# Kernel optimization log

Measured on AMD Instinct MI355X. Metric: run time of the kernel, lower is better.

The kernel has to match this reference:

```python
import jax, jax.numpy as jnp
import numpy as np

N_EMB = 1024
N_HEAD = 16
HEAD_DIM = N_EMB // N_HEAD


def setup_inputs() -> dict:
    key = jax.random.key(0)
    k_x, k_wa, k_ba, k_wp, k_bp = jax.random.split(key, 5)
    B, S = 4, 2048
    scale = 1.0 / np.sqrt(N_EMB)
    return {
        "x": jax.random.normal(k_x, (B, S, N_EMB), dtype=jnp.float32),
        "W_attn": jax.random.normal(k_wa, (N_EMB, 3 * N_EMB), dtype=jnp.float32) * scale,
        "b_attn": jax.random.normal(k_ba, (3 * N_EMB,), dtype=jnp.float32) * 0.01,
        "W_proj": jax.random.normal(k_wp, (N_EMB, N_EMB), dtype=jnp.float32) * scale,
        "b_proj": jax.random.normal(k_bp, (N_EMB,), dtype=jnp.float32) * 0.01,
    }


def _attention(x, W_attn, b_attn, W_proj, b_proj):
    B, S, E = x.shape
    qkv = x @ W_attn + b_attn  # [B, S, 3E]
    q, k, v = jnp.split(qkv, 3, axis=-1)
    # [B, H, S, D]
    q = q.reshape(B, S, N_HEAD, HEAD_DIM).transpose(0, 2, 1, 3)
    k = k.reshape(B, S, N_HEAD, HEAD_DIM).transpose(0, 2, 1, 3)
    v = v.reshape(B, S, N_HEAD, HEAD_DIM).transpose(0, 2, 1, 3)
    scores = jnp.einsum("bhqd,bhkd->bhqk", q, k) / jnp.sqrt(jnp.asarray(HEAD_DIM, x.dtype))
    causal = jnp.tril(jnp.ones((S, S), dtype=bool))
    scores = jnp.where(causal, scores, jnp.asarray(-jnp.inf, x.dtype))
    probs = jax.nn.softmax(scores, axis=-1)
    y = jnp.einsum("bhqk,bhkd->bhqd", probs, v)  # [B, H, S, D]
    y = y.transpose(0, 2, 1, 3).reshape(B, S, E)
    return y @ W_proj + b_proj


def reference(x, W_attn, b_attn, W_proj, b_proj):
    return _attention(x, W_attn, b_attn, W_proj, b_proj)
```

## Files before the change

### kernel.cpp

```cpp
#include <hip/hip_runtime.h>
#include <hip/hip_bf16.h>

typedef __bf16 bf16x8 __attribute__((ext_vector_type(8)));
typedef __bf16 bf16x4 __attribute__((ext_vector_type(4)));
typedef float f32x4 __attribute__((ext_vector_type(4)));

#define MFMA16(a, b, c) __builtin_amdgcn_mfma_f32_16x16x32_bf16(a, b, c, 0, 0, 0)

#define BATCH 4
#define SEQ   2048
#define EMB   1024
#define NHEAD 16
#define HDIM  64
#define ROWS  (BATCH * SEQ)
#define N_QKV (3 * EMB)
#define BH_STRIDE (SEQ * HDIM)

__device__ __forceinline__ void gload_lds16(const __bf16* gp, __bf16* lp) {
  __builtin_amdgcn_global_load_lds(
      (const __attribute__((address_space(1))) void*)gp,
      (__attribute__((address_space(3))) void*)lp, 16, 0, 0);
}

__global__ void cast_f32_to_bf16_x4(const float* __restrict__ src,
                                    __bf16* __restrict__ dst, int n4) {
  int i = blockIdx.x * blockDim.x + threadIdx.x;
  if (i >= n4) return;
  float4 f = ((const float4*)src)[i];
  bf16x4 o;
  o.x = (__bf16)f.x; o.y = (__bf16)f.y; o.z = (__bf16)f.z; o.w = (__bf16)f.w;
  ((bf16x4*)dst)[i] = o;
}

__global__ void transpose_to_bf16(const float* __restrict__ src,
                                  __bf16* __restrict__ dst, int R, int C) {
  __shared__ float t[32][33];
  int c0 = blockIdx.x * 32, r0 = blockIdx.y * 32;
  int tx = threadIdx.x, ty = threadIdx.y;
#pragma unroll
  for (int i = 0; i < 32; i += 8)
    t[ty + i][tx] = src[(size_t)(r0 + ty + i) * C + c0 + tx];
  __syncthreads();
#pragma unroll
  for (int i = 0; i < 32; i += 8)
    dst[(size_t)(c0 + ty + i) * R + r0 + tx] = (__bf16)t[tx][ty + i];
}

__global__ __launch_bounds__(256) void gemm_qkv(
    const __bf16* __restrict__ A, const __bf16* __restrict__ Bt,
    const float* __restrict__ bias,
    __bf16* __restrict__ Qt, __bf16* __restrict__ Kt, __bf16* __restrict__ Vt) {
  const int K = EMB;
  __shared__ __align__(16) __bf16 sA[128 * 32];
  __shared__ __align__(16) __bf16 sB[128 * 32];
  int id = blockIdx.x;
  int xcd = id & 7, j5 = id >> 3;
  int by = j5 >> 3;
  int bx = xcd * 8 + (j5 & 7);
  int m0 = by * 128, n0 = bx * 128;
  int tid = threadIdx.x;
  int wave = tid >> 6, lane = tid & 63;
  int wr = wave >> 1, wc = wave & 1;
  int l16 = lane & 15, quad = lane >> 4, quad4 = quad * 4;
  int f1 = tid * 8;
  int r1 = f1 >> 5, c1 = f1 & 31;
  int f2 = f1 + 2048;
  int r2 = f2 >> 5, c2 = f2 & 31;
  f32x4 acc[4][4] = {};
  for (int k0 = 0; k0 < K; k0 += 32) {
    gload_lds16(A + (size_t)(m0 + r1) * K + k0 + c1, &sA[wave * 512]);
    gload_lds16(A + (size_t)(m0 + r2) * K + k0 + c2, &sA[2048 + wave * 512]);
    gload_lds16(Bt + (size_t)(n0 + r1) * K + k0 + c1, &sB[wave * 512]);
    gload_lds16(Bt + (size_t)(n0 + r2) * K + k0 + c2, &sB[2048 + wave * 512]);
    __syncthreads();
    bf16x8 a[4], b[4];
#pragma unroll
    for (int i = 0; i < 4; i++)
      a[i] = *(const bf16x8*)(sA + (wr * 64 + i * 16 + l16) * 32 + quad * 8);
#pragma unroll
    for (int j = 0; j < 4; j++)
      b[j] = *(const bf16x8*)(sB + (wc * 64 + j * 16 + l16) * 32 + quad * 8);
#pragma unroll
    for (int i = 0; i < 4; i++)
#pragma unroll
      for (int j = 0; j < 4; j++) acc[i][j] = MFMA16(a[i], b[j], acc[i][j]);
    __syncthreads();
  }
  const float KSC = 0.18033688011112043f;
  int sec = m0 >> 10;
#pragma unroll
  for (int i = 0; i < 4; i++) {
    int e0 = m0 + wr * 64 + i * 16 + quad4;
    float4 bv4 = *(const float4*)(bias + e0);
    int h = (e0 & 1023) >> 6, d0 = e0 & 63;
#pragma unroll
    for (int j = 0; j < 4; j++) {
      int scol = n0 + wc * 64 + j * 16 + l16;
      int bidx = scol >> 11, s = scol & 2047;
      size_t base = (size_t)(bidx * NHEAD + h) * BH_STRIDE;
      float v0 = acc[i][j][0] + bv4.x;
      float v1 = acc[i][j][1] + bv4.y;
      float v2 = acc[i][j][2] + bv4.z;
      float v3 = acc[i][j][3] + bv4.w;
      if (sec == 0) {
        int idx = (s >> 4) * 1024 + (d0 >> 5) * 512 + ((d0 >> 3) & 3) * 128 +
                  (s & 15) * 8 + (d0 & 7);
        bf16x4 o4;
        o4.x = (__bf16)(v0 * KSC); o4.y = (__bf16)(v1 * KSC);
        o4.z = (__bf16)(v2 * KSC); o4.w = (__bf16)(v3 * KSC);
        *(bf16x4*)(Qt + base + idx) = o4;
      } else if (sec == 1) {
        int idx = (s >> 6) * 4096 + ((s >> 4) & 3) * 1024 + (d0 >> 5) * 512 +
                  ((d0 >> 3) & 3) * 128 + (s & 15) * 8 + (d0 & 7);
        bf16x4 o4;
        o4.x = (__bf16)v0; o4.y = (__bf16)v1;
        o4.z = (__bf16)v2; o4.w = (__bf16)v3;
        *(bf16x4*)(Kt + base + idx) = o4;
      } else {
        int idx = (s >> 6) * 4096 + (d0 >> 4) * 1024 + ((s >> 5) & 1) * 512 +
                  ((s >> 3) & 3) * 128 + (s & 7) + quad4 * 8;
        Vt[base + idx] = (__bf16)v0;
        Vt[base + idx + 8] = (__bf16)v1;
        Vt[base + idx + 16] = (__bf16)v2;
        Vt[base + idx + 24] = (__bf16)v3;
      }
    }
  }
}

#define PS2 68
__global__ __launch_bounds__(256, 4) void attn_fwd(
    const __bf16* __restrict__ Qt, const __bf16* __restrict__ Kt,
    const __bf16* __restrict__ Vt, __bf16* __restrict__ Y) {
  __shared__ __align__(16) __bf16 sK[4096];
  __shared__ __align__(16) __bf16 sV[4096];
  __shared__ __align__(16) __bf16 pbuf[4][32 * PS2];
  int id = blockIdx.x;
  int g = id >> 6;
  int gg = g & 3, sel = g >> 2;
  int qb = sel == 0 ? gg : sel == 1 ? 15 - gg : sel == 2 ? 4 + gg : 11 - gg;
  int hb = id & 63;
  int h = hb >> 2, b = hb & 3;
  int tid = threadIdx.x;
  int wave = tid >> 6, lane = tid & 63;
  int l16 = lane & 15, quad = lane >> 4, quad4 = quad * 4;
  int q0 = qb * 128;
  size_t bh = (size_t)b * NHEAD + h;
  const __bf16* Qh = Qt + bh * BH_STRIDE;
  const __bf16* Kh = Kt + bh * BH_STRIDE;
  const __bf16* Vh = Vt + bh * BH_STRIDE;
  int mq = q0 + wave * 32;
  const __bf16* qbase = Qh + (size_t)(mq >> 4) * 1024 + lane * 8;
  bf16x8 qa0 = *(const bf16x8*)(qbase);
  bf16x8 qa1 = *(const bf16x8*)(qbase + 512);
  bf16x8 qb0 = *(const bf16x8*)(qbase + 1024);
  bf16x8 qb1 = *(const bf16x8*)(qbase + 1536);
  f32x4 accA[4] = {}, accB[4] = {};
  float lA = 0.f, lB = 0.f;
  const float NEG_INF = -__builtin_inff();
  __bf16* pwA = pbuf[wave];
  __bf16* pwB = pbuf[wave] + 16 * PS2;
  int kt_end = q0 + 128;
  for (int kt = 0; kt < kt_end; kt += 64) {
    const __bf16* kg = Kh + (size_t)(kt >> 6) * 4096 + tid * 8;
    const __bf16* vg = Vh + (size_t)(kt >> 6) * 4096 + tid * 8;
    gload_lds16(kg, sK + tid * 8);
    gload_lds16(kg + 2048, sK + 2048 + tid * 8);
    gload_lds16(vg, sV + tid * 8);
    gload_lds16(vg + 2048, sV + 2048 + tid * 8);
    __syncthreads();
    bool diag = (kt + 64 > mq);
    int relA = mq + l16 - kt;
#pragma unroll
    for (int t = 0; t < 4; t++) {
      bf16x8 ka = *(const bf16x8*)(sK + t * 1024 + lane * 8);
      bf16x8 kb = *(const bf16x8*)(sK + t * 1024 + 512 + lane * 8);
      f32x4 zA = {}, zB = {};
      zA = MFMA16(ka, qa0, zA);
      zA = MFMA16(kb, qa1, zA);
      zB = MFMA16(ka, qb0, zB);
      zB = MFMA16(kb, qb1, zB);
      int kl = t * 16 + quad4;
      float pA[4], pB[4];
      if (diag) {
        int relB = relA + 16;
#pragma unroll
        for (int r = 0; r < 4; r++) {
          pA[r] = __builtin_amdgcn_exp2f(kl + r > relA ? NEG_INF : zA[r]);
          pB[r] = __builtin_amdgcn_exp2f(kl + r > relB ? NEG_INF : zB[r]);
        }
      } else {
#pragma unroll
        for (int r = 0; r < 4; r++) {
          pA[r] = __builtin_amdgcn_exp2f(zA[r]);
          pB[r] = __builtin_amdgcn_exp2f(zB[r]);
        }
      }
      lA += (pA[0] + pA[1]) + (pA[2] + pA[3]);
      lB += (pB[0] + pB[1]) + (pB[2] + pB[3]);
      bf16x4 oA, oB;
      oA.x = (__bf16)pA[0]; oA.y = (__bf16)pA[1];
      oA.z = (__bf16)pA[2]; oA.w = (__bf16)pA[3];
      oB.x = (__bf16)pB[0]; oB.y = (__bf16)pB[1];
      oB.z = (__bf16)pB[2]; oB.w = (__bf16)pB[3];
      *(bf16x4*)(pwA + l16 * PS2 + kl) = oA;
      *(bf16x4*)(pwB + l16 * PS2 + kl) = oB;
    }
    bf16x8 pA0 = *(const bf16x8*)(pwA + l16 * PS2 + quad * 8);
    bf16x8 pA1 = *(const bf16x8*)(pwA + l16 * PS2 + 32 + quad * 8);
    bf16x8 pB0 = *(const bf16x8*)(pwB + l16 * PS2 + quad * 8);
    bf16x8 pB1 = *(const bf16x8*)(pwB + l16 * PS2 + 32 + quad * 8);
#pragma unroll
    for (int jj = 0; jj < 4; jj++) {
      bf16x8 va = *(const bf16x8*)(sV + jj * 1024 + lane * 8);
      bf16x8 vb = *(const bf16x8*)(sV + jj * 1024 + 512 + lane * 8);
      accA[jj] = MFMA16(va, pA0, accA[jj]);
      accA[jj] = MFMA16(vb, pA1, accA[jj]);
      accB[jj] = MFMA16(va, pB0, accB[jj]);
      accB[jj] = MFMA16(vb, pB1, accB[jj]);
    }
    __syncthreads();
  }
  lA += __shfl_xor(lA, 16); lA += __shfl_xor(lA, 32);
  lB += __shfl_xor(lB, 16); lB += __shfl_xor(lB, 32);
  float invA = 1.f / lA, invB = 1.f / lB;
  int gqA = mq + l16, gqB = mq + 16 + l16;
#pragma unroll
  for (int jj = 0; jj < 4; jj++) {
    bf16x4 oA, oB;
    oA.x = (__bf16)(accA[jj][0] * invA);
    oA.y = (__bf16)(accA[jj][1] * invA);
    oA.z = (__bf16)(accA[jj][2] * invA);
    oA.w = (__bf16)(accA[jj][3] * invA);
    oB.x = (__bf16)(accB[jj][0] * invB);
    oB.y = (__bf16)(accB[jj][1] * invB);
    oB.z = (__bf16)(accB[jj][2] * invB);
    oB.w = (__bf16)(accB[jj][3] * invB);
    *(bf16x4*)(Y + ((size_t)b * SEQ + gqA) * EMB + h * HDIM + jj * 16 + quad4) = oA;
    *(bf16x4*)(Y + ((size_t)b * SEQ + gqB) * EMB + h * HDIM + jj * 16 + quad4) = oB;
  }
}

__global__ __launch_bounds__(256) void gemm_proj(
    const __bf16* __restrict__ A, const __bf16* __restrict__ Bt,
    const float* __restrict__ bias, float* __restrict__ out) {
  const int K = EMB;
  __shared__ __align__(16) __bf16 sA[128 * 32];
  __shared__ __align__(16) __bf16 sB[128 * 32];
  int id = blockIdx.x;
  int lid = (id & 7) * (512 >> 3) + (id >> 3);
  int bx = lid & 7, by = lid >> 3;
  int m0 = by * 128, n0 = bx * 128;
  int tid = threadIdx.x;
  int wave = tid >> 6, lane = tid & 63;
  int wr = wave >> 1, wc = wave & 1;
  int l16 = lane & 15, quad = lane >> 4;
  int f1 = tid * 8;
  int r1 = f1 >> 5, c1 = f1 & 31;
  int f2 = f1 + 2048;
  int r2 = f2 >> 5, c2 = f2 & 31;
  f32x4 acc[4][4] = {};
  for (int k0 = 0; k0 < K; k0 += 32) {
    gload_lds16(A + (size_t)(m0 + r1) * K + k0 + c1, &sA[wave * 512]);
    gload_lds16(A + (size_t)(m0 + r2) * K + k0 + c2, &sA[2048 + wave * 512]);
    gload_lds16(Bt + (size_t)(n0 + r1) * K + k0 + c1, &sB[wave * 512]);
    gload_lds16(Bt + (size_t)(n0 + r2) * K + k0 + c2, &sB[2048 + wave * 512]);
    __syncthreads();
    bf16x8 a[4], b[4];
#pragma unroll
    for (int i = 0; i < 4; i++)
      a[i] = *(const bf16x8*)(sA + (wr * 64 + i * 16 + l16) * 32 + quad * 8);
#pragma unroll
    for (int j = 0; j < 4; j++)
      b[j] = *(const bf16x8*)(sB + (wc * 64 + j * 16 + l16) * 32 + quad * 8);
#pragma unroll
    for (int i = 0; i < 4; i++)
#pragma unroll
      for (int j = 0; j < 4; j++) acc[i][j] = MFMA16(a[i], b[j], acc[i][j]);
    __syncthreads();
  }
#pragma unroll
  for (int i = 0; i < 4; i++) {
    int row = m0 + wr * 64 + i * 16 + quad * 4;
#pragma unroll
    for (int j = 0; j < 4; j++) {
      int col = n0 + wc * 64 + j * 16 + l16;
      float bv = bias[col];
#pragma unroll
      for (int r = 0; r < 4; r++)
        out[(size_t)(row + r) * EMB + col] = acc[i][j][r] + bv;
    }
  }
}

extern "C" void kernel_launch(void* const* d_in, const int* in_sizes, int n_in,
                              void* d_out, int out_size, void* d_ws, size_t ws_size,
                              hipStream_t stream) {
  const float* x      = (const float*)d_in[0];
  const float* W_attn = (const float*)d_in[1];
  const float* b_attn = (const float*)d_in[2];
  const float* W_proj = (const float*)d_in[3];
  const float* b_proj = (const float*)d_in[4];
  float* out = (float*)d_out;

  char* ws = (char*)d_ws;
  size_t off = 0;
  __bf16* xb   = (__bf16*)(ws + off); off += (size_t)ROWS * EMB * 2;
  __bf16* Wa_t = (__bf16*)(ws + off); off += (size_t)N_QKV * EMB * 2;
  __bf16* Wp_t = (__bf16*)(ws + off); off += (size_t)EMB * EMB * 2;
  __bf16* Qt   = (__bf16*)(ws + off); off += (size_t)ROWS * EMB * 2;
  __bf16* Kt   = (__bf16*)(ws + off); off += (size_t)ROWS * EMB * 2;
  __bf16* Vt   = (__bf16*)(ws + off); off += (size_t)ROWS * EMB * 2;
  __bf16* Yb   = (__bf16*)(ws + off); off += (size_t)ROWS * EMB * 2;

  {
    int n4 = ROWS * EMB / 4;
    cast_f32_to_bf16_x4<<<(n4 + 255) / 256, 256, 0, stream>>>(x, xb, n4);
    dim3 blk(32, 8);
    transpose_to_bf16<<<dim3(N_QKV / 32, EMB / 32), blk, 0, stream>>>(W_attn, Wa_t, EMB, N_QKV);
    transpose_to_bf16<<<dim3(EMB / 32, EMB / 32), blk, 0, stream>>>(W_proj, Wp_t, EMB, EMB);
  }
  gemm_qkv<<<dim3(1536), 256, 0, stream>>>(Wa_t, xb, b_attn, Qt, Kt, Vt);
  attn_fwd<<<dim3((SEQ / 128) * NHEAD * BATCH), 256, 0, stream>>>(Qt, Kt, Vt, Yb);
  gemm_proj<<<dim3(512), 256, 0, stream>>>(Yb, Wp_t, b_proj, out);
}
```

Baseline: 258.5 us.

## Double-buffer K/V tiles in attention and schedule longest query blocks first

The attention kernel now keeps two LDS buffers for K and V and prefetches the next tile asynchronously while the current tile is computed, with a single barrier per iteration. Block scheduling changes from an interleaved query-block order to a simple longest-first order (qb = 15 - g). Launch bounds drop from 4 to 3 blocks per CU to make room for the doubled LDS footprint. The trade is lower occupancy in exchange for hiding global-to-LDS load latency. There is also a possible race: the global_load_lds into the next buffer may not be waited on before the barrier, since the barrier may not drain vmcnt.

```diff
diff --git a/kernel.cpp b/kernel.cpp
--- a/kernel.cpp
+++ b/kernel.cpp
@@ -129,16 +129,15 @@
 }
 
 #define PS2 68
-__global__ __launch_bounds__(256, 4) void attn_fwd(
+__global__ __launch_bounds__(256, 3) void attn_fwd(
     const __bf16* __restrict__ Qt, const __bf16* __restrict__ Kt,
     const __bf16* __restrict__ Vt, __bf16* __restrict__ Y) {
-  __shared__ __align__(16) __bf16 sK[4096];
-  __shared__ __align__(16) __bf16 sV[4096];
+  __shared__ __align__(16) __bf16 sK[2][4096];
+  __shared__ __align__(16) __bf16 sV[2][4096];
   __shared__ __align__(16) __bf16 pbuf[4][32 * PS2];
   int id = blockIdx.x;
   int g = id >> 6;
-  int gg = g & 3, sel = g >> 2;
-  int qb = sel == 0 ? gg : sel == 1 ? 15 - gg : sel == 2 ? 4 + gg : 11 - gg;
+  int qb = 15 - g;
   int hb = id & 63;
   int h = hb >> 2, b = hb & 3;
   int tid = threadIdx.x;
@@ -160,21 +159,33 @@
   const float NEG_INF = -__builtin_inff();
   __bf16* pwA = pbuf[wave];
   __bf16* pwB = pbuf[wave] + 16 * PS2;
-  int kt_end = q0 + 128;
-  for (int kt = 0; kt < kt_end; kt += 64) {
-    const __bf16* kg = Kh + (size_t)(kt >> 6) * 4096 + tid * 8;
-    const __bf16* vg = Vh + (size_t)(kt >> 6) * 4096 + tid * 8;
-    gload_lds16(kg, sK + tid * 8);
-    gload_lds16(kg + 2048, sK + 2048 + tid * 8);
-    gload_lds16(vg, sV + tid * 8);
-    gload_lds16(vg + 2048, sV + 2048 + tid * 8);
-    __syncthreads();
+  int nt = (q0 + 128) >> 6;
+  gload_lds16(Kh + tid * 8, sK[0] + tid * 8);
+  gload_lds16(Kh + 2048 + tid * 8, sK[0] + 2048 + tid * 8);
+  gload_lds16(Vh + tid * 8, sV[0] + tid * 8);
+  gload_lds16(Vh + 2048 + tid * 8, sV[0] + 2048 + tid * 8);
+  __syncthreads();
+  int cur = 0;
+  for (int it = 0; it < nt; ++it) {
+    int kt = it * 64;
+    if (it + 1 < nt) {
+      const __bf16* kg = Kh + (size_t)(it + 1) * 4096 + tid * 8;
+      const __bf16* vg = Vh + (size_t)(it + 1) * 4096 + tid * 8;
+      __bf16* dK = sK[cur ^ 1] + tid * 8;
+      __bf16* dV = sV[cur ^ 1] + tid * 8;
+      gload_lds16(kg, dK);
+      gload_lds16(kg + 2048, dK + 2048);
+      gload_lds16(vg, dV);
+      gload_lds16(vg + 2048, dV + 2048);
+    }
+    const __bf16* sKc = sK[cur];
+    const __bf16* sVc = sV[cur];
     bool diag = (kt + 64 > mq);
     int relA = mq + l16 - kt;
 #pragma unroll
     for (int t = 0; t < 4; t++) {
-      bf16x8 ka = *(const bf16x8*)(sK + t * 1024 + lane * 8);
-      bf16x8 kb = *(const bf16x8*)(sK + t * 1024 + 512 + lane * 8);
+      bf16x8 ka = *(const bf16x8*)(sKc + t * 1024 + lane * 8);
+      bf16x8 kb = *(const bf16x8*)(sKc + t * 1024 + 512 + lane * 8);
       f32x4 zA = {}, zB = {};
       zA = MFMA16(ka, qa0, zA);
       zA = MFMA16(kb, qa1, zA);
@@ -212,14 +223,15 @@
     bf16x8 pB1 = *(const bf16x8*)(pwB + l16 * PS2 + 32 + quad * 8);
 #pragma unroll
     for (int jj = 0; jj < 4; jj++) {
-      bf16x8 va = *(const bf16x8*)(sV + jj * 1024 + lane * 8);
-      bf16x8 vb = *(const bf16x8*)(sV + jj * 1024 + 512 + lane * 8);
+      bf16x8 va = *(const bf16x8*)(sVc + jj * 1024 + lane * 8);
+      bf16x8 vb = *(const bf16x8*)(sVc + jj * 1024 + 512 + lane * 8);
       accA[jj] = MFMA16(va, pA0, accA[jj]);
       accA[jj] = MFMA16(vb, pA1, accA[jj]);
       accB[jj] = MFMA16(va, pB0, accB[jj]);
       accB[jj] = MFMA16(vb, pB1, accB[jj]);
     }
     __syncthreads();
+    cur ^= 1;
   }
   lA += __shfl_xor(lA, 16); lA += __shfl_xor(lA, 32);
   lB += __shfl_xor(lB, 16); lB += __shfl_xor(lB, 32);
```

After: 253.6 us. About the same (-1.9%).
